# Performance work log

Measured on AMD Instinct MI355X. Metric: run time of the kernel, lower is better.

The kernel has to match this reference:

```python
import jax, jax.numpy as jnp
import numpy as np

N = 100000   # nodes
E = 5000000  # edges (avg degree 50)
H = 16       # hidden dim


def gcn_conv(x, edge_index, edge_weight, W, b, num_nodes):
    """PyG GCNConv with edge weights: add self-loops (weight 1), symmetric
    normalization deg^-1/2 * w * deg^-1/2, linear transform, scatter-add."""
    row, col = edge_index[0], edge_index[1]  # source j -> target i
    loop = jnp.arange(num_nodes, dtype=edge_index.dtype)
    row = jnp.concatenate([row, loop])
    col = jnp.concatenate([col, loop])
    w = jnp.concatenate([edge_weight, jnp.ones((num_nodes,), edge_weight.dtype)])
    deg = jax.ops.segment_sum(w, col, num_segments=num_nodes)
    dinv = jnp.where(deg > 0, jax.lax.rsqrt(jnp.where(deg > 0, deg, 1.0)), 0.0)
    norm = dinv[row] * w * dinv[col]               # [E+N]
    h = x @ W                                      # [N, out]
    msg = norm[:, None] * h[row]                   # gather + scale
    out = jax.ops.segment_sum(msg, col, num_segments=num_nodes)  # scatter-add
    return out + b


def setup_inputs() -> dict:
    key = jax.random.key(0)
    k = jax.random.split(key, 7)
    x = jax.random.normal(k[0], (N, 1), dtype=jnp.float32)
    edge_index = jax.random.randint(k[1], (2, E), 0, N, dtype=jnp.int32)
    edge_attr = jax.random.uniform(k[2], (E,), dtype=jnp.float32)
    W1 = jax.random.normal(k[3], (1, H), dtype=jnp.float32) * (1.0 / np.sqrt(1.0))
    b1 = jnp.zeros((H,), dtype=jnp.float32)
    W2 = jax.random.normal(k[4], (H, 1), dtype=jnp.float32) * (1.0 / np.sqrt(H))
    b2 = jnp.zeros((1,), dtype=jnp.float32)
    return {"x": x, "edge_index": edge_index, "edge_attr": edge_attr,
            "W1": W1, "b1": b1, "W2": W2, "b2": b2}


def reference(x, edge_index, edge_attr, W1, b1, W2, b2):
    h = gcn_conv(x, edge_index, edge_attr, W1, b1, N)
    h = jax.nn.relu(h)
    out = gcn_conv(h, edge_index, edge_attr, W2, b2, N)
    return out
```

## Files before the change

### kernel.cpp

```cpp
#include <hip/hip_runtime.h>

#define THREADS 256
#define BSHIFT  12
#define BSIZE   4096
#define MAXNB   32
#define M       32
#define NREP    64
#define EPB     2048
#define EPT     (EPB / THREADS)

__global__ void k_count(const int* __restrict__ col, int* __restrict__ cur,
                        int2* __restrict__ hr, int E, int nb) {
    __shared__ int hist[MAXNB];
    int t = threadIdx.x;
    if (t < MAXNB) hist[t] = 0;
    __syncthreads();
    int base = blockIdx.x * EPB;
    bool full = (base + EPB <= E);
    if (full) {
#pragma unroll
        for (int k = 0; k < EPT / 4; ++k) {
            int4 c = *(const int4*)(col + base + (t + k * THREADS) * 4);
            atomicAdd(&hist[c.x >> BSHIFT], 1);
            atomicAdd(&hist[c.y >> BSHIFT], 1);
            atomicAdd(&hist[c.z >> BSHIFT], 1);
            atomicAdd(&hist[c.w >> BSHIFT], 1);
        }
    } else {
        for (int k = 0; k < EPT; ++k) {
            int e = base + t + k * THREADS;
            if (e < E) atomicAdd(&hist[col[e] >> BSHIFT], 1);
        }
    }
    __syncthreads();
    int rep = blockIdx.x & (NREP - 1);
    if (t < nb) {
        int rel = atomicAdd(&cur[t * NREP + rep], hist[t]);
        hr[blockIdx.x * MAXNB + t] = make_int2(hist[t], rel);
    }
}

__global__ void k_scan(const int* __restrict__ cnt, int* __restrict__ starts, int n) {
    __shared__ int tsum[THREADS];
    int t = threadIdx.x;
    int per = (n + THREADS - 1) / THREADS;
    int lo = t * per, hi = min(n, lo + per);
    int s = 0;
    for (int i = lo; i < hi; ++i) s += (cnt[i] + 3) & ~3;
    tsum[t] = s;
    __syncthreads();
    for (int d = 1; d < THREADS; d <<= 1) {
        int v = (t >= d) ? tsum[t - d] : 0;
        __syncthreads();
        tsum[t] += v;
        __syncthreads();
    }
    int base = (t > 0) ? tsum[t - 1] : 0;
    for (int i = lo; i < hi; ++i) { starts[i] = base; base += (cnt[i] + 3) & ~3; }
}

__global__ void k_scatter(const int* __restrict__ row, const int* __restrict__ col,
                          const float* __restrict__ w,
                          const int2* __restrict__ hr, const int* __restrict__ starts,
                          int2* __restrict__ rec, int E, int nb) {
    __shared__ int  lofs[MAXNB + 1];
    __shared__ int  rank[MAXNB];
    __shared__ int  rbase[MAXNB];
    __shared__ int2 buf[EPB];
    __shared__ unsigned char bkt[EPB];
    int t = threadIdx.x;
    if (t < MAXNB) rank[t] = 0;
    int rep = blockIdx.x & (NREP - 1);
    if (t < 64) {
        int h = 0, rel = 0;
        if (t < nb) {
            int2 v = hr[blockIdx.x * MAXNB + t];
            h = v.x; rel = v.y;
        }
        int inc = h;
#pragma unroll
        for (int d = 1; d < 32; d <<= 1) {
            int o = __shfl_up(inc, d, 64);
            if (t >= d) inc += o;
        }
        if (t == 0) lofs[0] = 0;
        if (t < nb) {
            lofs[t + 1] = inc;
            rbase[t] = starts[t * NREP + rep] + rel;
        }
    }
    __syncthreads();

    int base = blockIdx.x * EPB;
    bool full = (base + EPB <= E);
    if (full) {
#pragma unroll
        for (int k = 0; k < EPT / 4; ++k) {
            int idx = base + (t + k * THREADS) * 4;
            int4   c  = *(const int4*)(col + idx);
            int4   r  = *(const int4*)(row + idx);
            float4 wv = *(const float4*)(w + idx);
            int b, rk, pos;
            b = c.x >> BSHIFT; rk = atomicAdd(&rank[b], 1); pos = lofs[b] + rk;
            buf[pos] = make_int2(((c.x & (BSIZE-1)) << 17) | r.x, __float_as_int(wv.x));
            bkt[pos] = (unsigned char)b;
            b = c.y >> BSHIFT; rk = atomicAdd(&rank[b], 1); pos = lofs[b] + rk;
            buf[pos] = make_int2(((c.y & (BSIZE-1)) << 17) | r.y, __float_as_int(wv.y));
            bkt[pos] = (unsigned char)b;
            b = c.z >> BSHIFT; rk = atomicAdd(&rank[b], 1); pos = lofs[b] + rk;
            buf[pos] = make_int2(((c.z & (BSIZE-1)) << 17) | r.z, __float_as_int(wv.z));
            bkt[pos] = (unsigned char)b;
            b = c.w >> BSHIFT; rk = atomicAdd(&rank[b], 1); pos = lofs[b] + rk;
            buf[pos] = make_int2(((c.w & (BSIZE-1)) << 17) | r.w, __float_as_int(wv.w));
            bkt[pos] = (unsigned char)b;
        }
    } else {
        for (int k = 0; k < EPT; ++k) {
            int e = base + t + k * THREADS;
            if (e < E) {
                int c = col[e];
                int b = c >> BSHIFT;
                int rk = atomicAdd(&rank[b], 1);
                int pos = lofs[b] + rk;
                buf[pos] = make_int2(((c & (BSIZE-1)) << 17) | row[e], __float_as_int(w[e]));
                bkt[pos] = (unsigned char)b;
            }
        }
    }
    __syncthreads();

    int total = lofs[nb];
    for (int j = t; j < total; j += THREADS) {
        int b = bkt[j];
        rec[rbase[b] + (j - lofs[b])] = buf[j];
    }
}

template <bool HAS_SRC>
__global__ void k_acc(const int2* __restrict__ rec, const int* __restrict__ cnt,
                      const int* __restrict__ starts, const float* __restrict__ src,
                      float* __restrict__ part) {
    __shared__ float acc[BSIZE];
    int b = blockIdx.x / M, m = blockIdx.x % M;
    for (int j = threadIdx.x; j < BSIZE; j += THREADS) acc[j] = 0.0f;
    __syncthreads();
    const int4* rec4 = (const int4*)rec;
#pragma unroll
    for (int rr = 0; rr < NREP / M; ++rr) {
        int cell = b * NREP + m * (NREP / M) + rr;
        int lo = starts[cell];
        int hi = lo + cnt[cell];
        int i = lo + threadIdx.x * 8;
        for (; i + 7 < hi; i += THREADS * 8) {
            int4 q0 = rec4[(i >> 1) + 0];
            int4 q1 = rec4[(i >> 1) + 1];
            int4 q2 = rec4[(i >> 1) + 2];
            int4 q3 = rec4[(i >> 1) + 3];
            float v0 = __int_as_float(q0.y), v1 = __int_as_float(q0.w);
            float v2 = __int_as_float(q1.y), v3 = __int_as_float(q1.w);
            float v4 = __int_as_float(q2.y), v5 = __int_as_float(q2.w);
            float v6 = __int_as_float(q3.y), v7 = __int_as_float(q3.w);
            if (HAS_SRC) {
                v0 *= src[q0.x & 0x1FFFF]; v1 *= src[q0.z & 0x1FFFF];
                v2 *= src[q1.x & 0x1FFFF]; v3 *= src[q1.z & 0x1FFFF];
                v4 *= src[q2.x & 0x1FFFF]; v5 *= src[q2.z & 0x1FFFF];
                v6 *= src[q3.x & 0x1FFFF]; v7 *= src[q3.z & 0x1FFFF];
            }
            atomicAdd(&acc[((unsigned)q0.x) >> 17], v0);
            atomicAdd(&acc[((unsigned)q0.z) >> 17], v1);
            atomicAdd(&acc[((unsigned)q1.x) >> 17], v2);
            atomicAdd(&acc[((unsigned)q1.z) >> 17], v3);
            atomicAdd(&acc[((unsigned)q2.x) >> 17], v4);
            atomicAdd(&acc[((unsigned)q2.z) >> 17], v5);
            atomicAdd(&acc[((unsigned)q3.x) >> 17], v6);
            atomicAdd(&acc[((unsigned)q3.z) >> 17], v7);
        }
        for (; i < hi; ++i) {
            int2 r = rec[i];
            float v = __int_as_float(r.y);
            if (HAS_SRC) v *= src[r.x & 0x1FFFF];
            atomicAdd(&acc[((unsigned)r.x) >> 17], v);
        }
    }
    __syncthreads();
    float* dst = part + (size_t)blockIdx.x * BSIZE;
    for (int j = threadIdx.x; j < BSIZE; j += THREADS) dst[j] = acc[j];
}

__device__ __forceinline__ float reduceM(const float* __restrict__ part, int n) {
    int b = n >> BSHIFT, ofs = n & (BSIZE - 1);
    const float* pp = part + (size_t)b * M * BSIZE + ofs;
    float s = 0.0f;
#pragma unroll
    for (int m = 0; m < M; ++m) s += pp[(size_t)m * BSIZE];
    return s;
}

__global__ void k_red_dinv(const float* __restrict__ part, const float* __restrict__ x,
                           float* __restrict__ dinv, float* __restrict__ p, int N) {
    int i = blockIdx.x * blockDim.x + threadIdx.x;
    if (i < N) {
        float d  = reduceM(part, i) + 1.0f;
        float di = rsqrtf(d);
        dinv[i] = di;
        p[i] = di * x[i];
    }
}

__global__ void k_red_mlp(const float* __restrict__ part, const float* __restrict__ dinv,
                          const float* __restrict__ p,
                          const float* __restrict__ W1, const float* __restrict__ b1,
                          const float* __restrict__ W2,
                          float* __restrict__ q, int N) {
    int i = blockIdx.x * blockDim.x + threadIdx.x;
    if (i < N) {
        float di = dinv[i];
        float s  = di * reduceM(part, i) + di * p[i];
        float acc = 0.0f;
#pragma unroll
        for (int k = 0; k < 16; ++k) {
            float h = fmaxf(s * W1[k] + b1[k], 0.0f);
            acc += h * W2[k];
        }
        q[i] = di * acc;
    }
}

__global__ void k_red_out(const float* __restrict__ part, const float* __restrict__ dinv,
                          const float* __restrict__ q, const float* __restrict__ b2,
                          float* __restrict__ out, int N) {
    int i = blockIdx.x * blockDim.x + threadIdx.x;
    if (i < N) {
        float di = dinv[i];
        out[i] = di * reduceM(part, i) + di * q[i] + b2[0];
    }
}

extern "C" void kernel_launch(void* const* d_in, const int* in_sizes, int n_in,
                              void* d_out, int out_size, void* d_ws, size_t ws_size,
                              hipStream_t stream) {
    const float* x  = (const float*)d_in[0];
    const int*   ei = (const int*)  d_in[1];
    const float* ew = (const float*)d_in[2];
    const float* W1 = (const float*)d_in[3];
    const float* b1 = (const float*)d_in[4];
    const float* W2 = (const float*)d_in[5];
    const float* b2 = (const float*)d_in[6];

    const int N = in_sizes[0];
    const int E = in_sizes[2];
    const int* row = ei;
    const int* col = ei + E;
    const int nb = (N + BSIZE - 1) >> BSHIFT;
    const int eb = (E + EPB - 1) / EPB;

    char* wsp = (char*)d_ws;
    int2*  rec    = (int2*)wsp;   wsp += (size_t)E * 8 + 65536;
    float* part   = (float*)wsp;  wsp += (size_t)nb * M * BSIZE * 4;
    float* dinv   = (float*)wsp;  wsp += (size_t)N * 4;
    float* p      = (float*)wsp;  wsp += (size_t)N * 4;
    float* q      = (float*)wsp;  wsp += (size_t)N * 4;
    int2*  hr     = (int2*)wsp;   wsp += (size_t)eb * MAXNB * 8;
    int*   cur    = (int*)wsp;    wsp += (size_t)nb * NREP * 4;
    int*   starts = (int*)wsp;

    float* out = (float*)d_out;

    const int nbk = (N + THREADS - 1) / THREADS;
    const int ab  = nb * M;

    hipMemsetAsync(cur, 0, (size_t)nb * NREP * sizeof(int), stream);

    k_count  <<<eb, THREADS, 0, stream>>>(col, cur, hr, E, nb);
    k_scan   <<<1, THREADS, 0, stream>>>(cur, starts, nb * NREP);
    k_scatter<<<eb, THREADS, 0, stream>>>(row, col, ew, hr, starts, rec, E, nb);

    k_acc<false><<<ab, THREADS, 0, stream>>>(rec, cur, starts, nullptr, part);
    k_red_dinv  <<<nbk, THREADS, 0, stream>>>(part, x, dinv, p, N);

    k_acc<true><<<ab, THREADS, 0, stream>>>(rec, cur, starts, p, part);
    k_red_mlp  <<<nbk, THREADS, 0, stream>>>(part, dinv, p, W1, b1, W2, q, N);

    k_acc<true><<<ab, THREADS, 0, stream>>>(rec, cur, starts, q, part);
    k_red_out  <<<nbk, THREADS, 0, stream>>>(part, dinv, q, b2, out, N);
}
```

Before: 241.6 us.

## Replace atomic replica offsets with per-block count matrix and parallel scan

The bucketing pass no longer uses global atomics on replicated counters. Each edge block now writes its per-bucket histogram into a transposed count matrix, a per-bucket parallel scan computes deterministic block offsets, and scatter derives its write base from those offsets. The memset is dropped, and each accumulation block takes an equal contiguous chunk of its bucket rather than two replica cells, which evens out the load. The cost is a scan over every edge block per bucket and a small in-kernel prefix computation in each accumulation block.

After: 240.2 us. Within noise of the previous version (-0.6%).

```diff
diff --git a/kernel.cpp b/kernel.cpp
--- a/kernel.cpp
+++ b/kernel.cpp
@@ -1,26 +1,25 @@
 #include <hip/hip_runtime.h>
 
-#define THREADS 256
+#define T       256
 #define BSHIFT  12
 #define BSIZE   4096
 #define MAXNB   32
 #define M       32
-#define NREP    64
 #define EPB     2048
-#define EPT     (EPB / THREADS)
-
-__global__ void k_count(const int* __restrict__ col, int* __restrict__ cur,
-                        int2* __restrict__ hr, int E, int nb) {
+#define EPT     (EPB / T)
+
+__global__ void k_count(const int* __restrict__ col, int* __restrict__ cntT,
+                        int E, int nb, int ebp) {
     __shared__ int hist[MAXNB];
-    int t = threadIdx.x;
+    int t = threadIdx.x, g = blockIdx.x;
     if (t < MAXNB) hist[t] = 0;
     __syncthreads();
-    int base = blockIdx.x * EPB;
+    int base = g * EPB;
     bool full = (base + EPB <= E);
     if (full) {
 #pragma unroll
         for (int k = 0; k < EPT / 4; ++k) {
-            int4 c = *(const int4*)(col + base + (t + k * THREADS) * 4);
+            int4 c = *(const int4*)(col + base + (t + k * T) * 4);
             atomicAdd(&hist[c.x >> BSHIFT], 1);
             atomicAdd(&hist[c.y >> BSHIFT], 1);
             atomicAdd(&hist[c.z >> BSHIFT], 1);
@@ -28,99 +27,107 @@
         }
     } else {
         for (int k = 0; k < EPT; ++k) {
-            int e = base + t + k * THREADS;
+            int e = base + t + k * T;
             if (e < E) atomicAdd(&hist[col[e] >> BSHIFT], 1);
         }
     }
     __syncthreads();
-    int rep = blockIdx.x & (NREP - 1);
-    if (t < nb) {
-        int rel = atomicAdd(&cur[t * NREP + rep], hist[t]);
-        hr[blockIdx.x * MAXNB + t] = make_int2(hist[t], rel);
-    }
-}
-
-__global__ void k_scan(const int* __restrict__ cnt, int* __restrict__ starts, int n) {
-    __shared__ int tsum[THREADS];
-    int t = threadIdx.x;
-    int per = (n + THREADS - 1) / THREADS;
-    int lo = t * per, hi = min(n, lo + per);
-    int s = 0;
-    for (int i = lo; i < hi; ++i) s += (cnt[i] + 3) & ~3;
-    tsum[t] = s;
-    __syncthreads();
-    for (int d = 1; d < THREADS; d <<= 1) {
-        int v = (t >= d) ? tsum[t - d] : 0;
+    if (t < nb) cntT[t * ebp + g] = hist[t];
+}
+
+__global__ void k_scan(const int* __restrict__ cntT, int* __restrict__ ofsT,
+                       int* __restrict__ tot, int eb, int ebp) {
+    __shared__ int tsum[T];
+    __shared__ int carry;
+    int b = blockIdx.x, t = threadIdx.x;
+    if (t == 0) carry = 0;
+    __syncthreads();
+    int rounds = (eb + T - 1) / T;
+    for (int jr = 0; jr < rounds; ++jr) {
+        int idx = jr * T + t;
+        int v = (idx < eb) ? cntT[b * ebp + idx] : 0;
+        tsum[t] = v;
         __syncthreads();
-        tsum[t] += v;
+        for (int d = 1; d < T; d <<= 1) {
+            int o = (t >= d) ? tsum[t - d] : 0;
+            __syncthreads();
+            tsum[t] += o;
+            __syncthreads();
+        }
+        int excl = tsum[t] - v + carry;
+        if (idx < eb) ofsT[b * ebp + idx] = excl;
         __syncthreads();
-    }
-    int base = (t > 0) ? tsum[t - 1] : 0;
-    for (int i = lo; i < hi; ++i) { starts[i] = base; base += (cnt[i] + 3) & ~3; }
+        if (t == 0) carry += tsum[T - 1];
+        __syncthreads();
+    }
+    if (t == 0) tot[b] = carry;
 }
 
 __global__ void k_scatter(const int* __restrict__ row, const int* __restrict__ col,
                           const float* __restrict__ w,
-                          const int2* __restrict__ hr, const int* __restrict__ starts,
-                          int2* __restrict__ rec, int E, int nb) {
+                          const int* __restrict__ cntT, const int* __restrict__ ofsT,
+                          const int* __restrict__ tot,
+                          int2* __restrict__ rec, int E, int nb, int ebp) {
     __shared__ int  lofs[MAXNB + 1];
-    __shared__ int  rank[MAXNB];
+    __shared__ int  rnk[MAXNB];
     __shared__ int  rbase[MAXNB];
     __shared__ int2 buf[EPB];
     __shared__ unsigned char bkt[EPB];
-    int t = threadIdx.x;
-    if (t < MAXNB) rank[t] = 0;
-    int rep = blockIdx.x & (NREP - 1);
+    int t = threadIdx.x, g = blockIdx.x;
+    if (t < MAXNB) rnk[t] = 0;
     if (t < 64) {
-        int h = 0, rel = 0;
-        if (t < nb) {
-            int2 v = hr[blockIdx.x * MAXNB + t];
-            h = v.x; rel = v.y;
-        }
-        int inc = h;
+        int tv = (t < nb) ? ((tot[t] + 3) & ~3) : 0;
+        int incA = tv;
 #pragma unroll
         for (int d = 1; d < 32; d <<= 1) {
-            int o = __shfl_up(inc, d, 64);
-            if (t >= d) inc += o;
+            int o = __shfl_up(incA, d, 64);
+            if (t >= d) incA += o;
+        }
+        int h = (t < nb) ? cntT[t * ebp + g] : 0;
+        int incB = h;
+#pragma unroll
+        for (int d = 1; d < 32; d <<= 1) {
+            int o = __shfl_up(incB, d, 64);
+            if (t >= d) incB += o;
         }
         if (t == 0) lofs[0] = 0;
         if (t < nb) {
-            lofs[t + 1] = inc;
-            rbase[t] = starts[t * NREP + rep] + rel;
-        }
-    }
-    __syncthreads();
-
-    int base = blockIdx.x * EPB;
+            lofs[t + 1] = incB;
+            rbase[t] = (incA - tv) + ofsT[t * ebp + g];
+        }
+    }
+    __syncthreads();
+
+    int base = g * EPB;
     bool full = (base + EPB <= E);
     if (full) {
 #pragma unroll
         for (int k = 0; k < EPT / 4; ++k) {
-            int idx = base + (t + k * THREADS) * 4;
+            int idx = base + (t + k * T) * 4;
             int4   c  = *(const int4*)(col + idx);
             int4   r  = *(const int4*)(row + idx);
             float4 wv = *(const float4*)(w + idx);
             int b, rk, pos;
-            b = c.x >> BSHIFT; rk = atomicAdd(&rank[b], 1); pos = lofs[b] + rk;
+            b = c.x >> BSHIFT; rk = atomicAdd(&rnk[b], 1); pos = lofs[b] + rk;
             buf[pos] = make_int2(((c.x & (BSIZE-1)) << 17) | r.x, __float_as_int(wv.x));
             bkt[pos] = (unsigned char)b;
-            b = c.y >> BSHIFT; rk = atomicAdd(&rank[b], 1); pos = lofs[b] + rk;
+            b = c.y >> BSHIFT; rk = atomicAdd(&rnk[b], 1); pos = lofs[b] + rk;
             buf[pos] = make_int2(((c.y & (BSIZE-1)) << 17) | r.y, __float_as_int(wv.y));
             bkt[pos] = (unsigned char)b;
-            b = c.z >> BSHIFT; rk = atomicAdd(&rank[b], 1); pos = lofs[b] + rk;
+            b = c.z >> BSHIFT; rk = atomicAdd(&rnk[b], 1); pos = lofs[b] + rk;
             buf[pos] = make_int2(((c.z & (BSIZE-1)) << 17) | r.z, __float_as_int(wv.z));
             bkt[pos] = (unsigned char)b;
-            b = c.w >> BSHIFT; rk = atomicAdd(&rank[b], 1); pos = lofs[b] + rk;
+            b = c.w >> BSHIFT; rk = atomicAdd(&rnk[b], 1); pos = lofs[b] + rk;
             buf[pos] = make_int2(((c.w & (BSIZE-1)) << 17) | r.w, __float_as_int(wv.w));
             bkt[pos] = (unsigned char)b;
         }
     } else {
         for (int k = 0; k < EPT; ++k) {
-            int e = base + t + k * THREADS;
+            int e = base + t + k * T;
             if (e < E) {
                 int c = col[e];
                 int b = c >> BSHIFT;
-                int rk = atomicAdd(&rank[b], 1);
+                int rk = atomicAdd(&rnk[b], 1);
                 int pos = lofs[b] + rk;
                 buf[pos] = make_int2(((c & (BSIZE-1)) << 17) | row[e], __float_as_int(w[e]));
                 bkt[pos] = (unsigned char)b;
@@ -128,68 +135,77 @@
         }
     }
     __syncthreads();
-
     int total = lofs[nb];
-    for (int j = t; j < total; j += THREADS) {
+    for (int j = t; j < total; j += T) {
         int b = bkt[j];
         rec[rbase[b] + (j - lofs[b])] = buf[j];
     }
 }
 
 template <bool HAS_SRC>
-__global__ void k_acc(const int2* __restrict__ rec, const int* __restrict__ cnt,
-                      const int* __restrict__ starts, const float* __restrict__ src,
-                      float* __restrict__ part) {
+__global__ void k_acc(const int2* __restrict__ rec, const int* __restrict__ tot,
+                      const float* __restrict__ src, float* __restrict__ part, int nb) {
     __shared__ float acc[BSIZE];
-    int b = blockIdx.x / M, m = blockIdx.x % M;
-    for (int j = threadIdx.x; j < BSIZE; j += THREADS) acc[j] = 0.0f;
-    __syncthreads();
+    __shared__ int   bst[MAXNB];
+    int t = threadIdx.x, g = blockIdx.x;
+    int b = g / M, m = g % M;
+    if (t < 64) {
+        int tv = (t < nb) ? ((tot[t] + 3) & ~3) : 0;
+        int inc = tv;
+#pragma unroll
+        for (int d = 1; d < 32; d <<= 1) {
+            int o = __shfl_up(inc, d, 64);
+            if (t >= d) inc += o;
+        }
+        if (t < nb) bst[t] = inc - tv;
+    }
+    for (int j = t; j < BSIZE; j += T) acc[j] = 0.0f;
+    __syncthreads();
+    int s  = bst[b];
+    int tb = tot[b];
+    int chunk = ((tb + M - 1) / M + 7) & ~7;
+    int lo = s + m * chunk;
+    int hi = min(s + tb, lo + chunk);
     const int4* rec4 = (const int4*)rec;
-#pragma unroll
-    for (int rr = 0; rr < NREP / M; ++rr) {
-        int cell = b * NREP + m * (NREP / M) + rr;
-        int lo = starts[cell];
-        int hi = lo + cnt[cell];
-        int i = lo + threadIdx.x * 8;
-        for (; i + 7 < hi; i += THREADS * 8) {
-            int4 q0 = rec4[(i >> 1) + 0];
-            int4 q1 = rec4[(i >> 1) + 1];
-            int4 q2 = rec4[(i >> 1) + 2];
-            int4 q3 = rec4[(i >> 1) + 3];
-            float v0 = __int_as_float(q0.y), v1 = __int_as_float(q0.w);
-            float v2 = __int_as_float(q1.y), v3 = __int_as_float(q1.w);
-            float v4 = __int_as_float(q2.y), v5 = __int_as_float(q2.w);
-            float v6 = __int_as_float(q3.y), v7 = __int_as_float(q3.w);
-            if (HAS_SRC) {
-                v0 *= src[q0.x & 0x1FFFF]; v1 *= src[q0.z & 0x1FFFF];
-                v2 *= src[q1.x & 0x1FFFF]; v3 *= src[q1.z & 0x1FFFF];
-                v4 *= src[q2.x & 0x1FFFF]; v5 *= src[q2.z & 0x1FFFF];
-                v6 *= src[q3.x & 0x1FFFF]; v7 *= src[q3.z & 0x1FFFF];
-            }
-            atomicAdd(&acc[((unsigned)q0.x) >> 17], v0);
-            atomicAdd(&acc[((unsigned)q0.z) >> 17], v1);
-            atomicAdd(&acc[((unsigned)q1.x) >> 17], v2);
-            atomicAdd(&acc[((unsigned)q1.z) >> 17], v3);
-            atomicAdd(&acc[((unsigned)q2.x) >> 17], v4);
-            atomicAdd(&acc[((unsigned)q2.z) >> 17], v5);
-            atomicAdd(&acc[((unsigned)q3.x) >> 17], v6);
-            atomicAdd(&acc[((unsigned)q3.z) >> 17], v7);
-        }
-        for (; i < hi; ++i) {
-            int2 r = rec[i];
-            float v = __int_as_float(r.y);
-            if (HAS_SRC) v *= src[r.x & 0x1FFFF];
-            atomicAdd(&acc[((unsigned)r.x) >> 17], v);
-        }
-    }
-    __syncthreads();
-    float* dst = part + (size_t)blockIdx.x * BSIZE;
-    for (int j = threadIdx.x; j < BSIZE; j += THREADS) dst[j] = acc[j];
+    int i = lo + t * 8;
+    for (; i + 7 < hi; i += T * 8) {
+        int4 q0 = rec4[(i >> 1) + 0];
+        int4 q1 = rec4[(i >> 1) + 1];
+        int4 q2 = rec4[(i >> 1) + 2];
+        int4 q3 = rec4[(i >> 1) + 3];
+        float v0 = __int_as_float(q0.y), v1 = __int_as_float(q0.w);
+        float v2 = __int_as_float(q1.y), v3 = __int_as_float(q1.w);
+        float v4 = __int_as_float(q2.y), v5 = __int_as_float(q2.w);
+        float v6 = __int_as_float(q3.y), v7 = __int_as_float(q3.w);
+        if (HAS_SRC) {
+            v0 *= src[q0.x & 0x1FFFF]; v1 *= src[q0.z & 0x1FFFF];
+            v2 *= src[q1.x & 0x1FFFF]; v3 *= src[q1.z & 0x1FFFF];
+            v4 *= src[q2.x & 0x1FFFF]; v5 *= src[q2.z & 0x1FFFF];
+            v6 *= src[q3.x & 0x1FFFF]; v7 *= src[q3.z & 0x1FFFF];
+        }
+        atomicAdd(&acc[((unsigned)q0.x) >> 17], v0);
+        atomicAdd(&acc[((unsigned)q0.z) >> 17], v1);
+        atomicAdd(&acc[((unsigned)q1.x) >> 17], v2);
+        atomicAdd(&acc[((unsigned)q1.z) >> 17], v3);
+        atomicAdd(&acc[((unsigned)q2.x) >> 17], v4);
+        atomicAdd(&acc[((unsigned)q2.z) >> 17], v5);
+        atomicAdd(&acc[((unsigned)q3.x) >> 17], v6);
+        atomicAdd(&acc[((unsigned)q3.z) >> 17], v7);
+    }
+    for (; i < hi; ++i) {
+        int2 r = rec[i];
+        float v = __int_as_float(r.y);
+        if (HAS_SRC) v *= src[r.x & 0x1FFFF];
+        atomicAdd(&acc[((unsigned)r.x) >> 17], v);
+    }
+    __syncthreads();
+    float* dst = part + (size_t)g * BSIZE;
+    for (int j = t; j < BSIZE; j += T) dst[j] = acc[j];
 }
 
 __device__ __forceinline__ float reduceM(const float* __restrict__ part, int n) {
-    int b = n >> BSHIFT, ofs = n & (BSIZE - 1);
-    const float* pp = part + (size_t)b * M * BSIZE + ofs;
+    int b = n >> BSHIFT, o = n & (BSIZE - 1);
+    const float* pp = part + (size_t)b * M * BSIZE + o;
     float s = 0.0f;
 #pragma unroll
     for (int m = 0; m < M; ++m) s += pp[(size_t)m * BSIZE];
@@ -251,36 +267,38 @@
     const int E = in_sizes[2];
     const int* row = ei;
     const int* col = ei + E;
-    const int nb = (N + BSIZE - 1) >> BSHIFT;
-    const int eb = (E + EPB - 1) / EPB;
+    const int nb  = (N + BSIZE - 1) >> BSHIFT;
+    const int eb  = (E + EPB - 1) / EPB;
+    const int ebp = (eb + 63) & ~63;
 
     char* wsp = (char*)d_ws;
-    int2*  rec    = (int2*)wsp;   wsp += (size_t)E * 8 + 65536;
-    float* part   = (float*)wsp;  wsp += (size_t)nb * M * BSIZE * 4;
-    float* dinv   = (float*)wsp;  wsp += (size_t)N * 4;
-    float* p      = (float*)wsp;  wsp += (size_t)N * 4;
-    float* q      = (float*)wsp;  wsp += (size_t)N * 4;
-    int2*  hr     = (int2*)wsp;   wsp += (size_t)eb * MAXNB * 8;
-    int*   cur    = (int*)wsp;    wsp += (size_t)nb * NREP * 4;
-    int*   starts = (int*)wsp;
+    auto take = [&](size_t bytes) {
+        char* r = wsp; wsp += (bytes + 255) & ~(size_t)255; return (void*)r;
+    };
+    int2*  rec  = (int2*) take((size_t)(E + 4 * MAXNB) * 8);
+    float* part = (float*)take((size_t)nb * M * BSIZE * 4);
+    float* dinv = (float*)take((size_t)N * 4);
+    float* p    = (float*)take((size_t)N * 4);
+    float* q    = (float*)take((size_t)N * 4);
+    int*   cntT = (int*)  take((size_t)MAXNB * ebp * 4);
+    int*   ofsT = (int*)  take((size_t)MAXNB * ebp * 4);
+    int*   tot  = (int*)  take(MAXNB * 4);
 
     float* out = (float*)d_out;
 
-    const int nbk = (N + THREADS - 1) / THREADS;
+    const int nbk = (N + T - 1) / T;
     const int ab  = nb * M;
 
-    hipMemsetAsync(cur, 0, (size_t)nb * NREP * sizeof(int), stream);
-
-    k_count  <<<eb, THREADS, 0, stream>>>(col, cur, hr, E, nb);
-    k_scan   <<<1, THREADS, 0, stream>>>(cur, starts, nb * NREP);
-    k_scatter<<<eb, THREADS, 0, stream>>>(row, col, ew, hr, starts, rec, E, nb);
-
-    k_acc<false><<<ab, THREADS, 0, stream>>>(rec, cur, starts, nullptr, part);
-    k_red_dinv  <<<nbk, THREADS, 0, stream>>>(part, x, dinv, p, N);
-
-    k_acc<true><<<ab, THREADS, 0, stream>>>(rec, cur, starts, p, part);
-    k_red_mlp  <<<nbk, THREADS, 0, stream>>>(part, dinv, p, W1, b1, W2, q, N);
-
-    k_acc<true><<<ab, THREADS, 0, stream>>>(rec, cur, starts, q, part);
-    k_red_out  <<<nbk, THREADS, 0, stream>>>(part, dinv, q, b2, out, N);
-}
+    k_count  <<<eb, T, 0, stream>>>(col, cntT, E, nb, ebp);
+    k_scan   <<<nb, T, 0, stream>>>(cntT, ofsT, tot, eb, ebp);
+    k_scatter<<<eb, T, 0, stream>>>(row, col, ew, cntT, ofsT, tot, rec, E, nb, ebp);
+
+    k_acc<false><<<ab, T, 0, stream>>>(rec, tot, nullptr, part, nb);
+    k_red_dinv  <<<nbk, T, 0, stream>>>(part, x, dinv, p, N);
+
+    k_acc<true><<<ab, T, 0, stream>>>(rec, tot, p, part, nb);
+    k_red_mlp  <<<nbk, T, 0, stream>>>(part, dinv, p, W1, b1, W2, q, N);
+
+    k_acc<true><<<ab, T, 0, stream>>>(rec, tot, q, part, nb);
+    k_red_out  <<<nbk, T, 0, stream>>>(part, dinv, q, b2, out, N);
+}
```
